# Kernel tuning notes

Hardware: AMD Instinct MI355X
Metric: run time of the kernel (lower is better)

Reference implementation:

```python
import jax, jax.numpy as jnp
import numpy as np

B, NW, WL, CH, D, H, L, FF = 8, 1024, 8, 4, 512, 8, 4, 2048
K = 512  # num_masked = int(0.5 * NW)
SCALE = (D // H) ** -0.5


def _ln(x, g, b):
    m = jnp.mean(x, -1, keepdims=True)
    v = jnp.var(x, -1, keepdims=True)
    return (x - m) * jax.lax.rsqrt(v + 1e-5) * g + b


def setup_inputs():
    key = jax.random.key(0)
    ks = jax.random.split(key, 16)
    n = lambda i, shape, s=0.02: jax.random.normal(ks[i], shape, jnp.float32) * s
    return {
        "seq": jax.random.normal(ks[0], (B, NW * WL, CH), jnp.float32),
        "mask_idx": jax.lax.top_k(jax.random.uniform(ks[1], (B, NW)), K)[1].astype(jnp.int32),
        "pos_embedding": n(2, (1, NW + 1, D)),
        "mask_token": jax.random.normal(ks[3], (D,), jnp.float32),
        "pln1_g": jnp.ones((WL * CH,)), "pln1_b": jnp.zeros((WL * CH,)),
        "W_emb": n(4, (WL * CH, D)), "b_emb": jnp.zeros((D,)),
        "pln2_g": jnp.ones((D,)), "pln2_b": jnp.zeros((D,)),
        "aln_g": jnp.ones((L, D)), "aln_b": jnp.zeros((L, D)),
        "Wqkv": n(5, (L, D, 3 * D)),
        "Wo": n(6, (L, D, D)),
        "fln_g": jnp.ones((L, D)), "fln_b": jnp.zeros((L, D)),
        "Wff1": n(7, (L, D, FF)), "bff1": jnp.zeros((L, FF)),
        "Wff2": n(8, (L, FF, D)), "bff2": jnp.zeros((L, D)),
        "oln_g": jnp.ones((D,)), "oln_b": jnp.zeros((D,)),
        "W_words": n(9, (D, WL * CH)), "b_words": jnp.zeros((WL * CH,)),
    }


def reference(seq, mask_idx, pos_embedding, mask_token, pln1_g, pln1_b, W_emb, b_emb,
              pln2_g, pln2_b, aln_g, aln_b, Wqkv, Wo, fln_g, fln_b, Wff1, bff1,
              Wff2, bff2, oln_g, oln_b, W_words, b_words):
    b = seq.shape[0]
    words = seq.reshape(b, NW, WL * CH)                       # to_patch: 'b (n w) c -> b n (w c)'
    pos = pos_embedding[:, 1:NW + 1]                          # [1, NW, D]
    tokens = _ln(_ln(words, pln1_g, pln1_b) @ W_emb + b_emb, pln2_g, pln2_b) + pos
    mask_tokens = mask_token + pos                            # [1, NW, D] broadcast over batch
    bool_mask = jnp.zeros((b, NW), bool).at[jnp.arange(b)[:, None], mask_idx].set(True)
    tokens = jnp.where(bool_mask[..., None], mask_tokens, tokens)

    def block(x, p):
        h = _ln(x, p["ag"], p["ab"])
        q, k, v = [t.reshape(b, NW, H, D // H) for t in jnp.split(h @ p["Wqkv"], 3, axis=-1)]
        attn = jax.nn.softmax(jnp.einsum("bihd,bjhd->bhij", q, k) * SCALE, axis=-1)
        o = jnp.einsum("bhij,bjhd->bihd", attn, v).reshape(b, NW, D)
        x = x + o @ p["Wo"]
        h = _ln(x, p["fg"], p["fb"])
        x = x + jax.nn.gelu(h @ p["W1"] + p["b1"]) @ p["W2"] + p["b2"]
        return x, None

    layer_params = {"ag": aln_g, "ab": aln_b, "Wqkv": Wqkv, "Wo": Wo,
                    "fg": fln_g, "fb": fln_b, "W1": Wff1, "b1": bff1,
                    "W2": Wff2, "b2": bff2}
    encoded, _ = jax.lax.scan(block, tokens, layer_params)
    encoded = _ln(encoded, oln_g, oln_b)

    idx = mask_idx[..., None]
    enc_m = jnp.take_along_axis(encoded, idx, axis=1)         # [b, K, D] gather of masked positions
    pred = jax.nn.softmax((enc_m @ W_words + b_words).reshape(b, K, WL, CH), axis=-1)
    labels = jnp.take_along_axis(words, idx, axis=1).reshape(b, K, WL, CH)
    return pred, labels
```

## Files before the change

kernel.cpp:

```cpp
#include <hip/hip_runtime.h>
#include <hip/hip_bf16.h>
#include <stdint.h>


#define NTOK 8192
#define DMODEL 512
#define NHEAD 8
#define DHEAD 64
#define NWIN 1024
#define NBATCH 8
#define KMASK 512
#define FFDIM 2048
#define NLAYER 4

typedef __bf16 bf16x8 __attribute__((ext_vector_type(8)));
typedef float f32x4 __attribute__((ext_vector_type(4)));

#define MFMA16(a, b, c) __builtin_amdgcn_mfma_f32_16x16x32_bf16(a, b, c, 0, 0, 0)

static __device__ __forceinline__ void gload_lds16(const void* g, void* l) {
    __builtin_amdgcn_global_load_lds(
        (const __attribute__((address_space(1))) uint32_t*)g,
        (__attribute__((address_space(3))) uint32_t*)l, 16, 0, 0);
}

static __device__ __forceinline__ float gelu_tanh(float v) {
    float x3 = v * v * v;
    return 0.5f * v * (1.f + tanhf(0.7978845608028654f * (v + 0.044715f * x3)));
}

__global__ void embed_kernel(const float* __restrict__ seq,
                             const float* __restrict__ pos_emb,
                             const float* __restrict__ pln1_g,
                             const float* __restrict__ pln1_b,
                             const float* __restrict__ W_emb,
                             const float* __restrict__ b_emb,
                             const float* __restrict__ pln2_g,
                             const float* __restrict__ pln2_b,
                             float* __restrict__ x) {
    int tok = blockIdx.x;
    int w = tok & (NWIN - 1);
    int t = threadIdx.x;

    __shared__ float wraw[32];
    __shared__ float ln1[32];
    __shared__ float red[256], red2[256];

    if (t < 32) wraw[t] = seq[(size_t)tok * 32 + t];
    __syncthreads();

    float m = 0.f;
    for (int j = 0; j < 32; j++) m += wraw[j];
    m *= (1.f / 32.f);
    float v = 0.f;
    for (int j = 0; j < 32; j++) { float d = wraw[j] - m; v += d * d; }
    v *= (1.f / 32.f);
    float rs = rsqrtf(v + 1e-5f);
    if (t < 32) ln1[t] = (wraw[t] - m) * rs * pln1_g[t] + pln1_b[t];
    __syncthreads();

    int c0 = t, c1 = t + 256;
    float e0 = b_emb[c0];
    float e1 = b_emb[c1];
    for (int j = 0; j < 32; j++) {
        float a = ln1[j];
        e0 += a * W_emb[j * DMODEL + c0];
        e1 += a * W_emb[j * DMODEL + c1];
    }

    red[t] = e0 + e1;
    red2[t] = e0 * e0 + e1 * e1;
    __syncthreads();
    for (int o = 128; o > 0; o >>= 1) {
        if (t < o) { red[t] += red[t + o]; red2[t] += red2[t + o]; }
        __syncthreads();
    }
    float mean = red[0] * (1.f / 512.f);
    float var = red2[0] * (1.f / 512.f) - mean * mean;
    float rs2 = rsqrtf(var + 1e-5f);

    const float* pr = pos_emb + (size_t)(1 + w) * DMODEL;
    x[(size_t)tok * DMODEL + c0] =
        (e0 - mean) * rs2 * pln2_g[c0] + pln2_b[c0] + pr[c0];
    x[(size_t)tok * DMODEL + c1] =
        (e1 - mean) * rs2 * pln2_g[c1] + pln2_b[c1] + pr[c1];
}

__global__ void mask_scatter_kernel(const int* __restrict__ mask_idx,
                                    const float* __restrict__ mask_token,
                                    const float* __restrict__ pos_emb,
                                    float* __restrict__ x) {
    int bk = blockIdx.x;
    int b = bk >> 9;
    int k = bk & 511;
    int idx = mask_idx[b * KMASK + k];
    int t = threadIdx.x;
    float* row = x + (size_t)(b * NWIN + idx) * DMODEL;
    const float* pr = pos_emb + (size_t)(1 + idx) * DMODEL;
    row[t]       = mask_token[t]       + pr[t];
    row[t + 256] = mask_token[t + 256] + pr[t + 256];
}

__global__ void ln_kernel(const float* __restrict__ in,
                          __hip_bfloat16* __restrict__ out,
                          const float* __restrict__ g,
                          const float* __restrict__ bb) {
    int row = blockIdx.x;
    int t = threadIdx.x;
    const float* r = in + (size_t)row * DMODEL;
    float v0 = r[t], v1 = r[t + 256];
    __shared__ float red[256], red2[256];
    red[t] = v0 + v1;
    red2[t] = v0 * v0 + v1 * v1;
    __syncthreads();
    for (int o = 128; o > 0; o >>= 1) {
        if (t < o) { red[t] += red[t + o]; red2[t] += red2[t + o]; }
        __syncthreads();
    }
    float mean = red[0] * (1.f / 512.f);
    float var = red2[0] * (1.f / 512.f) - mean * mean;
    float rs = rsqrtf(var + 1e-5f);
    out[(size_t)row * DMODEL + t] =
        __float2bfloat16((v0 - mean) * rs * g[t] + bb[t]);
    out[(size_t)row * DMODEL + t + 256] =
        __float2bfloat16((v1 - mean) * rs * g[t + 256] + bb[t + 256]);
}

__global__ void wconv_kernel(const float* __restrict__ src,
                             __hip_bfloat16* __restrict__ dst,
                             int K, int N) {
    int l = blockIdx.z;
    src += (size_t)l * K * N;
    dst += (size_t)l * K * N;
    __shared__ float t[32][33];
    int n0 = blockIdx.x * 32, k0 = blockIdx.y * 32;
    int tx = threadIdx.x & 31, ty = threadIdx.x >> 5;
    for (int p = 0; p < 4; p++) {
        int k = k0 + ty + p * 8;
        t[ty + p * 8][tx] = src[(size_t)k * N + n0 + tx];
    }
    __syncthreads();
    for (int p = 0; p < 4; p++) {
        int n = n0 + ty + p * 8;
        dst[(size_t)n * K + k0 + tx] = __float2bfloat16(t[tx][ty + p * 8]);
    }
}

static __device__ __forceinline__ void epi_store128(
        const float* Cs, int c, int m0, int n0, int N, int tid,
        const float* bias, const float* resid,
        float* Cf, __hip_bfloat16* Cb, int act) {
    int rl = tid >> 3;
    int cb = (tid & 7) * 16;
    int grow = m0 + c * 32 + rl;
    size_t base = (size_t)grow * N + n0 + cb;
    if (Cf) {
        for (int q = 0; q < 4; q++) {
            float4 v = *(const float4*)&Cs[rl * 132 + cb + q * 4];
            float vv[4] = {v.x, v.y, v.z, v.w};
            float4 ov;
            float* op = (float*)&ov;
            for (int e = 0; e < 4; e++) {
                float u = vv[e];
                if (bias) u += bias[n0 + cb + q * 4 + e];
                if (act == 1) u = gelu_tanh(u);
                if (resid) u += resid[base + q * 4 + e];
                op[e] = u;
            }
            *(float4*)&Cf[base + q * 4] = ov;
        }
    } else {
        for (int half = 0; half < 2; half++) {
            union { uint4 u; __hip_bfloat16 h[8]; } pk;
            for (int e = 0; e < 8; e++) {
                float u = Cs[rl * 132 + cb + half * 8 + e];
                if (bias) u += bias[n0 + cb + half * 8 + e];
                if (act == 1) u = gelu_tanh(u);
                pk.h[e] = __float2bfloat16(u);
            }
            *(uint4*)&Cb[base + half * 8] = pk.u;
        }
    }
}

static __device__ __forceinline__ void epi_store64(
        const float* Cs, int c, int m0, int n0, int N, int tid,
        const float* bias, const float* resid,
        float* Cf, __hip_bfloat16* Cb, int act) {
    int rl = tid >> 3;
    int cb = (tid & 7) * 8;
    int grow = m0 + c * 32 + rl;
    size_t base = (size_t)grow * N + n0 + cb;
    if (Cf) {
        for (int q = 0; q < 2; q++) {
            float4 v = *(const float4*)&Cs[rl * 68 + cb + q * 4];
            float vv[4] = {v.x, v.y, v.z, v.w};
            float4 ov;
            float* op = (float*)&ov;
            for (int e = 0; e < 4; e++) {
                float u = vv[e];
                if (bias) u += bias[n0 + cb + q * 4 + e];
                if (act == 1) u = gelu_tanh(u);
                if (resid) u += resid[base + q * 4 + e];
                op[e] = u;
            }
            *(float4*)&Cf[base + q * 4] = ov;
        }
    } else {
        union { uint4 u; __hip_bfloat16 h[8]; } pk;
        for (int e = 0; e < 8; e++) {
            float u = Cs[rl * 68 + cb + e];
            if (bias) u += bias[n0 + cb + e];
            if (act == 1) u = gelu_tanh(u);
            pk.h[e] = __float2bfloat16(u);
        }
        *(uint4*)&Cb[base] = pk.u;
    }
}

#define PUT128(ACC, II, JJ)                                             \
    do {                                                                \
        int rb_ = (II) * 16 + quad * 4;                                 \
        int cc_ = wc * 64 + (JJ) * 16 + l16;                            \
        Cs[(rb_ + 0) * 132 + cc_] = (ACC)[0];                           \
        Cs[(rb_ + 1) * 132 + cc_] = (ACC)[1];                           \
        Cs[(rb_ + 2) * 132 + cc_] = (ACC)[2];                           \
        Cs[(rb_ + 3) * 132 + cc_] = (ACC)[3];                           \
    } while (0)

#define CHUNK128(C, A00, A01, A02, A03, A10, A11, A12, A13)             \
    do {                                                                \
        __syncthreads();                                                \
        if (wr == ((C) >> 1)) {                                         \
            PUT128(A00, 0, 0); PUT128(A01, 0, 1);                       \
            PUT128(A02, 0, 2); PUT128(A03, 0, 3);                       \
            PUT128(A10, 1, 0); PUT128(A11, 1, 1);                       \
            PUT128(A12, 1, 2); PUT128(A13, 1, 3);                       \
        }                                                               \
        __syncthreads();                                                \
        epi_store128(Cs, (C), m0, n0, N, tid, bias, resid, Cf, Cb, act);\
    } while (0)

__global__ __launch_bounds__(256) void mfma_gemm_kernel(
        const __hip_bfloat16* __restrict__ A,
        const __hip_bfloat16* __restrict__ Bt,
        const float* __restrict__ bias,
        const float* __restrict__ resid,
        float* __restrict__ Cf,
        __hip_bfloat16* __restrict__ Cb,
        int N, int K, int act, int ntile) {
    __shared__ __align__(16) char smem[16896];
    __hip_bfloat16* As = (__hip_bfloat16*)smem;
    __hip_bfloat16* Bs = (__hip_bfloat16*)(smem + 8192);
    float* Cs = (float*)smem;

    int tid = threadIdx.x;
    int wave = tid >> 6, lane = tid & 63;
    int quad = lane >> 4, l16 = lane & 15;
    int wr = wave >> 1, wc = wave & 1;

    int id = blockIdx.x;
    int slot = id >> 3;
    int mt = (id & 7) * 8 + slot / ntile;
    int nt = slot - (slot / ntile) * ntile;
    int m0 = mt * 128, n0 = nt * 128;

    f32x4 zero = {0.f, 0.f, 0.f, 0.f};
    f32x4 acc00 = zero, acc01 = zero, acc02 = zero, acc03 = zero;
    f32x4 acc10 = zero, acc11 = zero, acc12 = zero, acc13 = zero;
    f32x4 acc20 = zero, acc21 = zero, acc22 = zero, acc23 = zero;
    f32x4 acc30 = zero, acc31 = zero, acc32 = zero, acc33 = zero;

    int rsub = lane >> 2, csub = lane & 3;

    for (int k0 = 0; k0 < K; k0 += 32) {
        for (int p = 0; p < 2; p++) {
            int row = wave * 32 + p * 16;
            const char* ga = (const char*)A +
                (size_t)(m0 + row + rsub) * (K * 2) + k0 * 2 + csub * 16;
            gload_lds16(ga, &As[row * 32]);
            const char* gb = (const char*)Bt +
                (size_t)(n0 + row + rsub) * (K * 2) + k0 * 2 + csub * 16;
            gload_lds16(gb, &Bs[row * 32]);
        }
        __syncthreads();

        bf16x8 a0 = *(const bf16x8*)&As[(wr * 64 +  0 + l16) * 32 + quad * 8];
        bf16x8 a1 = *(const bf16x8*)&As[(wr * 64 + 16 + l16) * 32 + quad * 8];
        bf16x8 a2 = *(const bf16x8*)&As[(wr * 64 + 32 + l16) * 32 + quad * 8];
        bf16x8 a3 = *(const bf16x8*)&As[(wr * 64 + 48 + l16) * 32 + quad * 8];
        bf16x8 b0 = *(const bf16x8*)&Bs[(wc * 64 +  0 + l16) * 32 + quad * 8];
        bf16x8 b1 = *(const bf16x8*)&Bs[(wc * 64 + 16 + l16) * 32 + quad * 8];
        bf16x8 b2 = *(const bf16x8*)&Bs[(wc * 64 + 32 + l16) * 32 + quad * 8];
        bf16x8 b3 = *(const bf16x8*)&Bs[(wc * 64 + 48 + l16) * 32 + quad * 8];

        acc00 = MFMA16(a0, b0, acc00); acc01 = MFMA16(a0, b1, acc01);
        acc02 = MFMA16(a0, b2, acc02); acc03 = MFMA16(a0, b3, acc03);
        acc10 = MFMA16(a1, b0, acc10); acc11 = MFMA16(a1, b1, acc11);
        acc12 = MFMA16(a1, b2, acc12); acc13 = MFMA16(a1, b3, acc13);
        acc20 = MFMA16(a2, b0, acc20); acc21 = MFMA16(a2, b1, acc21);
        acc22 = MFMA16(a2, b2, acc22); acc23 = MFMA16(a2, b3, acc23);
        acc30 = MFMA16(a3, b0, acc30); acc31 = MFMA16(a3, b1, acc31);
        acc32 = MFMA16(a3, b2, acc32); acc33 = MFMA16(a3, b3, acc33);
        __syncthreads();
    }

    CHUNK128(0, acc00, acc01, acc02, acc03, acc10, acc11, acc12, acc13);
    CHUNK128(1, acc20, acc21, acc22, acc23, acc30, acc31, acc32, acc33);
    CHUNK128(2, acc00, acc01, acc02, acc03, acc10, acc11, acc12, acc13);
    CHUNK128(3, acc20, acc21, acc22, acc23, acc30, acc31, acc32, acc33);
}

#define PUT64(ACC, II, JJ)                                              \
    do {                                                                \
        int rb_ = (II) * 16 + quad * 4;                                 \
        int cc_ = (JJ) * 16 + l16;                                      \
        Cs[(rb_ + 0) * 68 + cc_] = (ACC)[0];                            \
        Cs[(rb_ + 1) * 68 + cc_] = (ACC)[1];                            \
        Cs[(rb_ + 2) * 68 + cc_] = (ACC)[2];                            \
        Cs[(rb_ + 3) * 68 + cc_] = (ACC)[3];                            \
    } while (0)

#define CHUNK64(C)                                                      \
    do {                                                                \
        __syncthreads();                                                \
        if (wave == (C)) {                                              \
            PUT64(acc00, 0, 0); PUT64(acc01, 0, 1);                     \
            PUT64(acc02, 0, 2); PUT64(acc03, 0, 3);                     \
            PUT64(acc10, 1, 0); PUT64(acc11, 1, 1);                     \
            PUT64(acc12, 1, 2); PUT64(acc13, 1, 3);                     \
        }                                                               \
        __syncthreads();                                                \
        epi_store64(Cs, (C), m0, n0, N, tid, bias, resid, Cf, Cb, act); \
    } while (0)

__global__ __launch_bounds__(256) void mfma_gemm_n64_kernel(
        const __hip_bfloat16* __restrict__ A,
        const __hip_bfloat16* __restrict__ Bt,
        const float* __restrict__ bias,
        const float* __restrict__ resid,
        float* __restrict__ Cf,
        __hip_bfloat16* __restrict__ Cb,
        int N, int K, int act, int ntile) {
    __shared__ __align__(16) char smem[12288];
    __hip_bfloat16* As = (__hip_bfloat16*)smem;
    __hip_bfloat16* Bs = (__hip_bfloat16*)(smem + 8192);
    float* Cs = (float*)smem;

    int tid = threadIdx.x;
    int wave = tid >> 6, lane = tid & 63;
    int quad = lane >> 4, l16 = lane & 15;

    int id = blockIdx.x;
    int slot = id >> 3;
    int mt = (id & 7) * 8 + slot / ntile;
    int nt = slot - (slot / ntile) * ntile;
    int m0 = mt * 128, n0 = nt * 64;

    f32x4 zero = {0.f, 0.f, 0.f, 0.f};
    f32x4 acc00 = zero, acc01 = zero, acc02 = zero, acc03 = zero;
    f32x4 acc10 = zero, acc11 = zero, acc12 = zero, acc13 = zero;

    int rsub = lane >> 2, csub = lane & 3;

    for (int k0 = 0; k0 < K; k0 += 32) {
        for (int p = 0; p < 2; p++) {
            int row = wave * 32 + p * 16;
            const char* ga = (const char*)A +
                (size_t)(m0 + row + rsub) * (K * 2) + k0 * 2 + csub * 16;
            gload_lds16(ga, &As[row * 32]);
        }
        {
            int row = wave * 16;
            const char* gb = (const char*)Bt +
                (size_t)(n0 + row + rsub) * (K * 2) + k0 * 2 + csub * 16;
            gload_lds16(gb, &Bs[row * 32]);
        }
        __syncthreads();

        bf16x8 a0 = *(const bf16x8*)&As[(wave * 32 +  0 + l16) * 32 + quad * 8];
        bf16x8 a1 = *(const bf16x8*)&As[(wave * 32 + 16 + l16) * 32 + quad * 8];
        bf16x8 b0 = *(const bf16x8*)&Bs[( 0 + l16) * 32 + quad * 8];
        bf16x8 b1 = *(const bf16x8*)&Bs[(16 + l16) * 32 + quad * 8];
        bf16x8 b2 = *(const bf16x8*)&Bs[(32 + l16) * 32 + quad * 8];
        bf16x8 b3 = *(const bf16x8*)&Bs[(48 + l16) * 32 + quad * 8];

        acc00 = MFMA16(a0, b0, acc00); acc01 = MFMA16(a0, b1, acc01);
        acc02 = MFMA16(a0, b2, acc02); acc03 = MFMA16(a0, b3, acc03);
        acc10 = MFMA16(a1, b0, acc10); acc11 = MFMA16(a1, b1, acc11);
        acc12 = MFMA16(a1, b2, acc12); acc13 = MFMA16(a1, b3, acc13);
        __syncthreads();
    }

    CHUNK64(0);
    CHUNK64(1);
    CHUNK64(2);
    CHUNK64(3);
}

#define KP 72
__global__ __launch_bounds__(256) void attn_mfma_kernel(
        const __hip_bfloat16* __restrict__ qkv,
        __hip_bfloat16* __restrict__ o) {
    int id = blockIdx.x;
    int slot = id >> 3;
    int bh = (id & 7) * 8 + (slot >> 3);
    int itile = slot & 7;
    int b = bh >> 3, hh = bh & 7;

    int tid = threadIdx.x;
    int wave = tid >> 6, lane = tid & 63;
    int quad = lane >> 4, l16 = lane & 15;
    int i0 = itile * 128;

    __shared__ __align__(16) __hip_bfloat16 Ks[64 * KP];
    __shared__ __align__(16) __hip_bfloat16 Vt[64 * KP];
    __shared__ __align__(16) __hip_bfloat16 Ps[4][16 * KP];

    bf16x8 aq[2][2];
#pragma unroll
    for (int g = 0; g < 2; g++) {
        const __hip_bfloat16* qrow =
            qkv + (size_t)(b * NWIN + i0 + g * 64 + wave * 16 + l16) * 1536 + hh * 64;
        aq[g][0] = *(const bf16x8*)(qrow + quad * 8);
        aq[g][1] = *(const bf16x8*)(qrow + 32 + quad * 8);
    }

    float lp[2][4];
    f32x4 acc[2][4];
    f32x4 zero = {0.f, 0.f, 0.f, 0.f};
#pragma unroll
    for (int g = 0; g < 2; g++)
#pragma unroll
        for (int n = 0; n < 4; n++) { acc[g][n] = zero; lp[g][n] = 0.f; }

    for (int kt = 0; kt < 16; kt++) {
        int k0 = kt * 64;
        __syncthreads();

#pragma unroll
        for (int p = 0; p < 2; p++) {
            int f = p * 256 + tid;
            int r = f >> 3;
            int j = f & 7;
            int c8 = j * 8;
            const __hip_bfloat16* kp =
                qkv + (size_t)(b * NWIN + k0 + r) * 1536 + 512 + hh * 64 + c8;
            *(uint4*)&Ks[r * KP + c8] = *(const uint4*)kp;
            union { uint4 u; __hip_bfloat16 h[8]; } vv;
            vv.u = *(const uint4*)(qkv + (size_t)(b * NWIN + k0 + r) * 1536 +
                                   1024 + hh * 64 + c8);
            int colb = (((r >> 3) ^ j) << 3) + (r & 7);
#pragma unroll
            for (int u = 0; u < 8; u++) Vt[(c8 + u) * KP + colb] = vv.h[u];
        }
        __syncthreads();

        bf16x8 bk[4][2], bv[4][2];
#pragma unroll
        for (int n = 0; n < 4; n++) {
            int key = n * 16 + l16;
            bk[n][0] = *(const bf16x8*)&Ks[key * KP + quad * 8];
            bk[n][1] = *(const bf16x8*)&Ks[key * KP + 32 + quad * 8];
            int d = n * 16 + l16;
            int sw = (d >> 3) & 7;
            bv[n][0] = *(const bf16x8*)&Vt[d * KP + ((quad ^ sw) << 3)];
            bv[n][1] = *(const bf16x8*)&Vt[d * KP + (((quad + 4) ^ sw) << 3)];
        }

#pragma unroll
        for (int g = 0; g < 2; g++) {
            f32x4 s[4];
#pragma unroll
            for (int n = 0; n < 4; n++) {
                f32x4 t = zero;
                t = MFMA16(aq[g][0], bk[n][0], t);
                t = MFMA16(aq[g][1], bk[n][1], t);
                s[n] = t;
            }
#pragma unroll
            for (int r = 0; r < 4; r++) {
                float ls = 0.f;
#pragma unroll
                for (int n = 0; n < 4; n++) {
                    float pv = __expf(s[n][r] * 0.125f);
                    Ps[wave][(quad * 4 + r) * KP + n * 16 + l16] =
                        __float2bfloat16(pv);
                    ls += pv;
                }
                lp[g][r] += ls;
            }
            bf16x8 ap0 = *(const bf16x8*)&Ps[wave][l16 * KP + quad * 8];
            bf16x8 ap1 = *(const bf16x8*)&Ps[wave][l16 * KP + 32 + quad * 8];
#pragma unroll
            for (int n = 0; n < 4; n++) {
                acc[g][n] = MFMA16(ap0, bv[n][0], acc[g][n]);
                acc[g][n] = MFMA16(ap1, bv[n][1], acc[g][n]);
            }
        }
    }

#pragma unroll
    for (int g = 0; g < 2; g++) {
#pragma unroll
        for (int r = 0; r < 4; r++) {
            float ls = lp[g][r];
            ls += __shfl_xor(ls, 1);
            ls += __shfl_xor(ls, 2);
            ls += __shfl_xor(ls, 4);
            ls += __shfl_xor(ls, 8);
            float invl = 1.f / ls;
            int row = i0 + g * 64 + wave * 16 + quad * 4 + r;
#pragma unroll
            for (int n = 0; n < 4; n++) {
                o[(size_t)(b * NWIN + row) * DMODEL + hh * 64 + n * 16 + l16] =
                    __float2bfloat16(acc[g][n][r] * invl);
            }
        }
    }
}

__global__ void out_kernel(const float* __restrict__ x,
                           const int* __restrict__ mask_idx,
                           const float* __restrict__ oln_g,
                           const float* __restrict__ oln_b,
                           const float* __restrict__ W_words,
                           const float* __restrict__ b_words,
                           const float* __restrict__ seq,
                           float* __restrict__ out) {
    int k = blockIdx.x, b = blockIdx.y;
    int idx = mask_idx[b * KMASK + k];
    int t = threadIdx.x;
    const float* row = x + (size_t)(b * NWIN + idx) * DMODEL;
    float v0 = row[t], v1 = row[t + 256];

    __shared__ float red[256], red2[256];
    __shared__ float sh[512];
    __shared__ float part[256];
    __shared__ float lg[32];

    red[t] = v0 + v1;
    red2[t] = v0 * v0 + v1 * v1;
    __syncthreads();
    for (int o = 128; o > 0; o >>= 1) {
        if (t < o) { red[t] += red[t + o]; red2[t] += red2[t + o]; }
        __syncthreads();
    }
    float mean = red[0] * (1.f / 512.f);
    float var = red2[0] * (1.f / 512.f) - mean * mean;
    float rs = rsqrtf(var + 1e-5f);
    sh[t]       = (v0 - mean) * rs * oln_g[t] + oln_b[t];
    sh[t + 256] = (v1 - mean) * rs * oln_g[t + 256] + oln_b[t + 256];
    __syncthreads();

    int c = t & 31, ch = t >> 5;
    float p = 0.f;
    for (int j = ch * 64; j < ch * 64 + 64; j++)
        p += sh[j] * W_words[j * 32 + c];
    part[t] = p;
    __syncthreads();
    if (t < 32) {
        float s = b_words[t];
        for (int u = 0; u < 8; u++) s += part[u * 32 + t];
        lg[t] = s;
    }
    __syncthreads();

    size_t obase = (size_t)(b * KMASK + k) * 32;
    if (t < 32) {
        int g0 = t & ~3;
        float mx = fmaxf(fmaxf(lg[g0], lg[g0 + 1]), fmaxf(lg[g0 + 2], lg[g0 + 3]));
        float s = expf(lg[g0] - mx) + expf(lg[g0 + 1] - mx) +
                  expf(lg[g0 + 2] - mx) + expf(lg[g0 + 3] - mx);
        out[obase + t] = expf(lg[t] - mx) / s;
        out[131072 + obase + t] = seq[(size_t)b * 32768 + (size_t)idx * 32 + t];
    }
}

extern "C" void kernel_launch(void* const* d_in, const int* in_sizes, int n_in,
                              void* d_out, int out_size, void* d_ws, size_t ws_size,
                              hipStream_t stream) {
    const float* seq      = (const float*)d_in[0];
    const int*   mask_idx = (const int*)d_in[1];
    const float* pos_emb  = (const float*)d_in[2];
    const float* mask_tok = (const float*)d_in[3];
    const float* pln1_g   = (const float*)d_in[4];
    const float* pln1_b   = (const float*)d_in[5];
    const float* W_emb    = (const float*)d_in[6];
    const float* b_emb    = (const float*)d_in[7];
    const float* pln2_g   = (const float*)d_in[8];
    const float* pln2_b   = (const float*)d_in[9];
    const float* aln_g    = (const float*)d_in[10];
    const float* aln_b    = (const float*)d_in[11];
    const float* Wqkv     = (const float*)d_in[12];
    const float* Wo       = (const float*)d_in[13];
    const float* fln_g    = (const float*)d_in[14];
    const float* fln_b    = (const float*)d_in[15];
    const float* Wff1     = (const float*)d_in[16];
    const float* bff1     = (const float*)d_in[17];
    const float* Wff2     = (const float*)d_in[18];
    const float* bff2     = (const float*)d_in[19];
    const float* oln_g    = (const float*)d_in[20];
    const float* oln_b    = (const float*)d_in[21];
    const float* W_words  = (const float*)d_in[22];
    const float* b_words  = (const float*)d_in[23];

    uint8_t* ws = (uint8_t*)d_ws;
    float* x = (float*)ws;
    __hip_bfloat16* qkv_bf = (__hip_bfloat16*)(ws + 16777216);
    __hip_bfloat16* ff_bf  = qkv_bf;
    __hip_bfloat16* h_bf   = (__hip_bfloat16*)(ws + 50331648);
    __hip_bfloat16* o_bf   = (__hip_bfloat16*)(ws + 58720256);
    __hip_bfloat16* wqkv_t = (__hip_bfloat16*)(ws + 67108864);
    __hip_bfloat16* wo_t   = wqkv_t + (size_t)NLAYER * DMODEL * 3 * DMODEL;
    __hip_bfloat16* wff1_t = wo_t   + (size_t)NLAYER * DMODEL * DMODEL;
    __hip_bfloat16* wff2_t = wff1_t + (size_t)NLAYER * DMODEL * FFDIM;

    wconv_kernel<<<dim3(48, 16, NLAYER), 256, 0, stream>>>(Wqkv, wqkv_t, DMODEL, 3 * DMODEL);
    wconv_kernel<<<dim3(16, 16, NLAYER), 256, 0, stream>>>(Wo,   wo_t,   DMODEL, DMODEL);
    wconv_kernel<<<dim3(64, 16, NLAYER), 256, 0, stream>>>(Wff1, wff1_t, DMODEL, FFDIM);
    wconv_kernel<<<dim3(16, 64, NLAYER), 256, 0, stream>>>(Wff2, wff2_t, FFDIM, DMODEL);

    embed_kernel<<<NTOK, 256, 0, stream>>>(seq, pos_emb, pln1_g, pln1_b,
                                           W_emb, b_emb, pln2_g, pln2_b, x);
    mask_scatter_kernel<<<NBATCH * KMASK, 256, 0, stream>>>(mask_idx, mask_tok, pos_emb, x);

    for (int l = 0; l < NLAYER; l++) {
        ln_kernel<<<NTOK, 256, 0, stream>>>(x, h_bf, aln_g + l * DMODEL, aln_b + l * DMODEL);
        mfma_gemm_kernel<<<64 * 12, 256, 0, stream>>>(
            h_bf, wqkv_t + (size_t)l * DMODEL * 3 * DMODEL,
            nullptr, nullptr, nullptr, qkv_bf, 3 * DMODEL, DMODEL, 0, 12);
        attn_mfma_kernel<<<512, 256, 0, stream>>>(qkv_bf, o_bf);
        mfma_gemm_n64_kernel<<<64 * 8, 256, 0, stream>>>(
            o_bf, wo_t + (size_t)l * DMODEL * DMODEL,
            nullptr, x, x, nullptr, DMODEL, DMODEL, 0, 8);
        ln_kernel<<<NTOK, 256, 0, stream>>>(x, h_bf, fln_g + l * DMODEL, fln_b + l * DMODEL);
        mfma_gemm_kernel<<<64 * 16, 256, 0, stream>>>(
            h_bf, wff1_t + (size_t)l * DMODEL * FFDIM,
            bff1 + (size_t)l * FFDIM, nullptr, nullptr, ff_bf, FFDIM, DMODEL, 1, 16);
        mfma_gemm_n64_kernel<<<64 * 8, 256, 0, stream>>>(
            ff_bf, wff2_t + (size_t)l * FFDIM * DMODEL,
            bff2 + (size_t)l * DMODEL, x, x, nullptr, DMODEL, FFDIM, 0, 8);
    }

    out_kernel<<<dim3(KMASK, NBATCH), 256, 0, stream>>>(
        x, mask_idx, oln_g, oln_b, W_words, b_words, seq, (float*)d_out);
}
```

Measured before the change: 1.026 ms.

## Double-buffer LDS tiles in GEMM kernels to overlap global loads with MFMA

Both GEMM kernels now use two LDS stage buffers. The next K-slice is loaded with global_load_lds while MFMAs run on the current one, and the trailing barrier per iteration is dropped. This hides global memory latency and halves the number of barriers. It doubles LDS usage per block, which may lower occupancy.

```diff
diff --git a/kernel.cpp b/kernel.cpp
--- a/kernel.cpp
+++ b/kernel.cpp
@@ -241,6 +241,20 @@
         epi_store128(Cs, (C), m0, n0, N, tid, bias, resid, Cf, Cb, act);\
     } while (0)
 
+#define STAGE128(K0, BUF)                                               \
+    do {                                                                \
+        char* as_ = smem + (BUF) * 16384;                               \
+        char* bs_ = as_ + 8192;                                         \
+        _Pragma("unroll")                                               \
+        for (int p_ = 0; p_ < 2; p_++) {                                \
+            int row_ = wave * 32 + p_ * 16;                             \
+            gload_lds16(Abase + (size_t)(p_ * 16) * (K * 2) + (K0) * 2, \
+                        as_ + row_ * 64);                               \
+            gload_lds16(Bbase + (size_t)(p_ * 16) * (K * 2) + (K0) * 2, \
+                        bs_ + row_ * 64);                               \
+        }                                                               \
+    } while (0)
+
 __global__ __launch_bounds__(256) void mfma_gemm_kernel(
         const __hip_bfloat16* __restrict__ A,
         const __hip_bfloat16* __restrict__ Bt,
@@ -249,9 +263,7 @@
         float* __restrict__ Cf,
         __hip_bfloat16* __restrict__ Cb,
         int N, int K, int act, int ntile) {
-    __shared__ __align__(16) char smem[16896];
-    __hip_bfloat16* As = (__hip_bfloat16*)smem;
-    __hip_bfloat16* Bs = (__hip_bfloat16*)(smem + 8192);
+    __shared__ __align__(16) char smem[32768];
     float* Cs = (float*)smem;
 
     int tid = threadIdx.x;
@@ -272,27 +284,29 @@
     f32x4 acc30 = zero, acc31 = zero, acc32 = zero, acc33 = zero;
 
     int rsub = lane >> 2, csub = lane & 3;
-
-    for (int k0 = 0; k0 < K; k0 += 32) {
-        for (int p = 0; p < 2; p++) {
-            int row = wave * 32 + p * 16;
-            const char* ga = (const char*)A +
-                (size_t)(m0 + row + rsub) * (K * 2) + k0 * 2 + csub * 16;
-            gload_lds16(ga, &As[row * 32]);
-            const char* gb = (const char*)Bt +
-                (size_t)(n0 + row + rsub) * (K * 2) + k0 * 2 + csub * 16;
-            gload_lds16(gb, &Bs[row * 32]);
-        }
+    const char* Abase = (const char*)A +
+        (size_t)(m0 + wave * 32 + rsub) * (K * 2) + csub * 16;
+    const char* Bbase = (const char*)Bt +
+        (size_t)(n0 + wave * 32 + rsub) * (K * 2) + csub * 16;
+
+    int nit = K >> 5;
+    STAGE128(0, 0);
+    for (int it = 0; it < nit; it++) {
         __syncthreads();
-
-        bf16x8 a0 = *(const bf16x8*)&As[(wr * 64 +  0 + l16) * 32 + quad * 8];
-        bf16x8 a1 = *(const bf16x8*)&As[(wr * 64 + 16 + l16) * 32 + quad * 8];
-        bf16x8 a2 = *(const bf16x8*)&As[(wr * 64 + 32 + l16) * 32 + quad * 8];
-        bf16x8 a3 = *(const bf16x8*)&As[(wr * 64 + 48 + l16) * 32 + quad * 8];
-        bf16x8 b0 = *(const bf16x8*)&Bs[(wc * 64 +  0 + l16) * 32 + quad * 8];
-        bf16x8 b1 = *(const bf16x8*)&Bs[(wc * 64 + 16 + l16) * 32 + quad * 8];
-        bf16x8 b2 = *(const bf16x8*)&Bs[(wc * 64 + 32 + l16) * 32 + quad * 8];
-        bf16x8 b3 = *(const bf16x8*)&Bs[(wc * 64 + 48 + l16) * 32 + quad * 8];
+        if (it + 1 < nit) STAGE128((it + 1) << 5, (it + 1) & 1);
+
+        const __hip_bfloat16* as =
+            (const __hip_bfloat16*)(smem + (it & 1) * 16384);
+        const __hip_bfloat16* bs = as + 4096;
+
+        bf16x8 a0 = *(const bf16x8*)&as[(wr * 64 +  0 + l16) * 32 + quad * 8];
+        bf16x8 a1 = *(const bf16x8*)&as[(wr * 64 + 16 + l16) * 32 + quad * 8];
+        bf16x8 a2 = *(const bf16x8*)&as[(wr * 64 + 32 + l16) * 32 + quad * 8];
+        bf16x8 a3 = *(const bf16x8*)&as[(wr * 64 + 48 + l16) * 32 + quad * 8];
+        bf16x8 b0 = *(const bf16x8*)&bs[(wc * 64 +  0 + l16) * 32 + quad * 8];
+        bf16x8 b1 = *(const bf16x8*)&bs[(wc * 64 + 16 + l16) * 32 + quad * 8];
+        bf16x8 b2 = *(const bf16x8*)&bs[(wc * 64 + 32 + l16) * 32 + quad * 8];
+        bf16x8 b3 = *(const bf16x8*)&bs[(wc * 64 + 48 + l16) * 32 + quad * 8];
 
         acc00 = MFMA16(a0, b0, acc00); acc01 = MFMA16(a0, b1, acc01);
         acc02 = MFMA16(a0, b2, acc02); acc03 = MFMA16(a0, b3, acc03);
@@ -302,7 +316,6 @@
         acc22 = MFMA16(a2, b2, acc22); acc23 = MFMA16(a2, b3, acc23);
         acc30 = MFMA16(a3, b0, acc30); acc31 = MFMA16(a3, b1, acc31);
         acc32 = MFMA16(a3, b2, acc32); acc33 = MFMA16(a3, b3, acc33);
-        __syncthreads();
     }
 
     CHUNK128(0, acc00, acc01, acc02, acc03, acc10, acc11, acc12, acc13);
@@ -334,6 +347,19 @@
         epi_store64(Cs, (C), m0, n0, N, tid, bias, resid, Cf, Cb, act); \
     } while (0)
 
+#define STAGE64(K0, BUF)                                                \
+    do {                                                                \
+        char* as_ = smem + (BUF) * 12288;                               \
+        char* bs_ = as_ + 8192;                                         \
+        _Pragma("unroll")                                               \
+        for (int p_ = 0; p_ < 2; p_++) {                                \
+            int row_ = wave * 32 + p_ * 16;                             \
+            gload_lds16(Abase + (size_t)(p_ * 16) * (K * 2) + (K0) * 2, \
+                        as_ + row_ * 64);                               \
+        }                                                               \
+        gload_lds16(Bbase + (K0) * 2, bs_ + (wave * 16) * 64);          \
+    } while (0)
+
 __global__ __launch_bounds__(256) void mfma_gemm_n64_kernel(
         const __hip_bfloat16* __restrict__ A,
         const __hip_bfloat16* __restrict__ Bt,
@@ -342,9 +368,7 @@
         float* __restrict__ Cf,
         __hip_bfloat16* __restrict__ Cb,
         int N, int K, int act, int ntile) {
-    __shared__ __align__(16) char smem[12288];
-    __hip_bfloat16* As = (__hip_bfloat16*)smem;
-    __hip_bfloat16* Bs = (__hip_bfloat16*)(smem + 8192);
+    __shared__ __align__(16) char smem[24576];
     float* Cs = (float*)smem;
 
     int tid = threadIdx.x;
@@ -362,34 +386,32 @@
     f32x4 acc10 = zero, acc11 = zero, acc12 = zero, acc13 = zero;
 
     int rsub = lane >> 2, csub = lane & 3;
-
-    for (int k0 = 0; k0 < K; k0 += 32) {
-        for (int p = 0; p < 2; p++) {
-            int row = wave * 32 + p * 16;
-            const char* ga = (const char*)A +
-                (size_t)(m0 + row + rsub) * (K * 2) + k0 * 2 + csub * 16;
-            gload_lds16(ga, &As[row * 32]);
-        }
-        {
-            int row = wave * 16;
-            const char* gb = (const char*)Bt +
-                (size_t)(n0 + row + rsub) * (K * 2) + k0 * 2 + csub * 16;
-            gload_lds16(gb, &Bs[row * 32]);
-        }
+    const char* Abase = (const char*)A +
+        (size_t)(m0 + wave * 32 + rsub) * (K * 2) + csub * 16;
+    const char* Bbase = (const char*)Bt +
+        (size_t)(n0 + wave * 16 + rsub) * (K * 2) + csub * 16;
+
+    int nit = K >> 5;
+    STAGE64(0, 0);
+    for (int it = 0; it < nit; it++) {
         __syncthreads();
-
-        bf16x8 a0 = *(const bf16x8*)&As[(wave * 32 +  0 + l16) * 32 + quad * 8];
-        bf16x8 a1 = *(const bf16x8*)&As[(wave * 32 + 16 + l16) * 32 + quad * 8];
-        bf16x8 b0 = *(const bf16x8*)&Bs[( 0 + l16) * 32 + quad * 8];
-        bf16x8 b1 = *(const bf16x8*)&Bs[(16 + l16) * 32 + quad * 8];
-        bf16x8 b2 = *(const bf16x8*)&Bs[(32 + l16) * 32 + quad * 8];
-        bf16x8 b3 = *(const bf16x8*)&Bs[(48 + l16) * 32 + quad * 8];
+        if (it + 1 < nit) STAGE64((it + 1) << 5, (it + 1) & 1);
+
+        const __hip_bfloat16* as =
+            (const __hip_bfloat16*)(smem + (it & 1) * 12288);
+        const __hip_bfloat16* bs = as + 4096;
+
+        bf16x8 a0 = *(const bf16x8*)&as[(wave * 32 +  0 + l16) * 32 + quad * 8];
+        bf16x8 a1 = *(const bf16x8*)&as[(wave * 32 + 16 + l16) * 32 + quad * 8];
+        bf16x8 b0 = *(const bf16x8*)&bs[( 0 + l16) * 32 + quad * 8];
+        bf16x8 b1 = *(const bf16x8*)&bs[(16 + l16) * 32 + quad * 8];
+        bf16x8 b2 = *(const bf16x8*)&bs[(32 + l16) * 32 + quad * 8];
+        bf16x8 b3 = *(const bf16x8*)&bs[(48 + l16) * 32 + quad * 8];
 
         acc00 = MFMA16(a0, b0, acc00); acc01 = MFMA16(a0, b1, acc01);
         acc02 = MFMA16(a0, b2, acc02); acc03 = MFMA16(a0, b3, acc03);
         acc10 = MFMA16(a1, b0, acc10); acc11 = MFMA16(a1, b1, acc11);
         acc12 = MFMA16(a1, b2, acc12); acc13 = MFMA16(a1, b3, acc13);
-        __syncthreads();
     }
 
     CHUNK64(0);
```

Result: faster. 897.9 us (-12.5%).
